# Performance work log

Measured on AMD Instinct MI355X. Metric: run time of the kernel, lower is better.

## Reference

```python
import jax, jax.numpy as jnp
import numpy as np


def setup_inputs() -> dict:
    key = jax.random.key(0)
    k1, k2 = jax.random.split(key)
    b, n, d = 8, 4096, 512
    num_codebooks, codebook_size = 1, 8192
    x = jax.random.normal(k1, (b, n, d), dtype=jnp.float32)
    embed = jax.random.normal(k2, (num_codebooks, codebook_size, d), dtype=jnp.float32)
    return {"x": x, "embed": embed}


def reference(x, embed):
    # Eval-mode forward of EuclideanCodebook (temperature 0 -> argmax of -cdist).
    # x: [b, n, d]; embed: [h, C, d] with h = num_codebooks = 1.
    b, n, d = x.shape
    h, C, _ = embed.shape
    flatten = x.reshape(h, b * n, d)                       # h * d packing (h=1)

    # dist = -cdist(flatten, embed): negative euclidean distance [h, N, C]
    x2 = jnp.sum(flatten * flatten, axis=-1, keepdims=True)   # [h, N, 1]
    e2 = jnp.sum(embed * embed, axis=-1)[:, None, :]          # [h, 1, C]
    xe = jnp.einsum('hnd,hcd->hnc', flatten, embed)           # [h, N, C]
    d2 = jnp.clip(x2 + e2 - 2.0 * xe, 0.0)
    dist = -jnp.sqrt(d2)                                      # [h, N, C]

    # gumbel_sample at temp 0 / eval -> straight argmax
    embed_ind_flat = jnp.argmax(dist, axis=-1)                # [h, N]

    # quantize = batched_embedding(embed_ind, embed): gather codes
    quantize = jnp.take_along_axis(embed, embed_ind_flat[..., None], axis=1)  # [h, N, d]

    # unpack + drop the codebook dim (needs_codebook_dim path)
    quantize = quantize.reshape(b, n, d)
    embed_ind = embed_ind_flat.reshape(b, n)
    dist = dist.reshape(h, b, n, C)  # dist keeps the codebook dim, as in source
    return quantize, embed_ind, dist
```

## Files before the change

kernel.cpp:

```cpp
#include <hip/hip_runtime.h>
#include <hip/hip_fp16.h>
#include <stdint.h>

typedef _Float16 f16x8 __attribute__((ext_vector_type(8)));
typedef _Float16 f16x4 __attribute__((ext_vector_type(4)));
typedef float    f32x4 __attribute__((ext_vector_type(4)));

static constexpr int NROWS = 32768;
static constexpr int NCODE = 8192;
static constexpr int DDIM  = 512;
static constexpr int BM = 256, BN = 256, BK = 64;
static constexpr int NBM = NROWS / BM;
static constexpr int NBN = NCODE / BN;
static constexpr int NPART = NBN * 2;

static constexpr size_t OFF_IND  = (size_t)NROWS * DDIM;
static constexpr size_t OFF_DIST = OFF_IND + NROWS;

static constexpr size_t WS_XH   = 0;
static constexpr size_t WS_XL   = WS_XH + (size_t)NROWS * DDIM * 2;
static constexpr size_t WS_EH   = WS_XL + (size_t)NROWS * DDIM * 2;
static constexpr size_t WS_EL   = WS_EH + (size_t)NCODE * DDIM * 2;
static constexpr size_t WS_X2   = WS_EL + (size_t)NCODE * DDIM * 2;
static constexpr size_t WS_E2   = WS_X2 + (size_t)NROWS * 4;
static constexpr size_t WS_PART = WS_E2 + (size_t)NCODE * 4;

__device__ inline void gload_lds16(const void* g, void* l) {
  __builtin_amdgcn_global_load_lds((const __attribute__((address_space(1))) void*)g,
                                   (__attribute__((address_space(3))) void*)l,
                                   16, 0, 0);
}

__global__ __launch_bounds__(128)
void prep_kernel(const float* __restrict__ x, const float* __restrict__ e,
                 _Float16* __restrict__ xh, _Float16* __restrict__ xl,
                 _Float16* __restrict__ eh, _Float16* __restrict__ el,
                 float* __restrict__ x2, float* __restrict__ e2)
{
  int bid = blockIdx.x;
  const float* src; _Float16 *dh, *dl; float* nrm;
  if (bid < NROWS) {
    src = x + (size_t)bid * DDIM;
    dh = xh + (size_t)bid * DDIM;  dl = xl + (size_t)bid * DDIM;
    nrm = x2 + bid;
  } else {
    int r = bid - NROWS;
    src = e + (size_t)r * DDIM;
    dh = eh + (size_t)r * DDIM;    dl = el + (size_t)r * DDIM;
    nrm = e2 + r;
  }
  int t = threadIdx.x;
  float4 v = reinterpret_cast<const float4*>(src)[t];
  double s = (double)v.x*v.x + (double)v.y*v.y + (double)v.z*v.z + (double)v.w*v.w;
  f16x4 h, l;
  h.x = (_Float16)v.x; l.x = (_Float16)(v.x - (float)h.x);
  h.y = (_Float16)v.y; l.y = (_Float16)(v.y - (float)h.y);
  h.z = (_Float16)v.z; l.z = (_Float16)(v.z - (float)h.z);
  h.w = (_Float16)v.w; l.w = (_Float16)(v.w - (float)h.w);
  reinterpret_cast<f16x4*>(dh)[t] = h;
  reinterpret_cast<f16x4*>(dl)[t] = l;
  #pragma unroll
  for (int m = 1; m < 64; m <<= 1) s += __shfl_xor(s, m);
  __shared__ double sh[2];
  if ((t & 63) == 0) sh[t >> 6] = s;
  __syncthreads();
  if (t == 0) nrm[0] = (float)(sh[0] + sh[1]);
}

__global__ __launch_bounds__(512, 2)
void dist_gemm_kernel(const _Float16* __restrict__ xh, const _Float16* __restrict__ xl,
                      const _Float16* __restrict__ eh, const _Float16* __restrict__ el,
                      const float* __restrict__ x2, const float* __restrict__ e2,
                      float* __restrict__ dist, float2* __restrict__ part)
{
  __shared__ _Float16 L[2][2][BM * BK];

  const int tid  = threadIdx.x;
  const int wid  = tid >> 6;
  const int lane = tid & 63;
  const int qwr  = wid >> 1;
  const int qwc  = wid & 1;

  const int flat = blockIdx.x;
  const int swz  = (flat & 7) * (int)(gridDim.x >> 3) + (flat >> 3);
  const int bm = swz >> 5;
  const int bn = swz & 31;
  const int R  = bm * BM;
  const int Cc = bn * BN;

  const int l3 = lane >> 3;
  const int l7 = lane & 7;
  const int srcslot = ((l7 ^ l3) << 4);

  auto STAGE = [&](int t, int nb) {
    const _Float16* As = (t < 16) ? xh : xl;
    const _Float16* Bs = (t < 8 || t >= 16) ? eh : el;
    const int k0b = (t & 7) * (BK * 2);
    #pragma unroll
    for (int h = 0; h < 2; ++h) {
      #pragma unroll
      for (int g = 0; g < 2; ++g) {
        const int r = h * 128 + g * 64 + wid * 8 + l3;
        gload_lds16((const char*)As + (size_t)(R + r) * (DDIM * 2) + k0b + srcslot,
                    &L[nb][0][(h * 128 + g * 64 + wid * 8) * BK]);
        gload_lds16((const char*)Bs + (size_t)(Cc + r) * (DDIM * 2) + k0b + srcslot,
                    &L[nb][1][(h * 128 + g * 64 + wid * 8) * BK]);
      }
    }
  };

  const int l15   = lane & 15;
  const int kslot = (lane >> 4) << 4;

  auto LDA = [&](f16x8 (&af)[2][2], int b, int mq) {
    #pragma unroll
    for (int m = 0; m < 2; ++m)
      #pragma unroll
      for (int ks = 0; ks < 2; ++ks) {
        const int row = mq * 128 + qwr * 32 + m * 16 + l15;
        const int kb  = (ks * 64 + kslot) ^ ((row & 7) << 4);
        af[m][ks] = *(const f16x8*)((const char*)&L[b][0][0] + row * 128 + kb);
      }
  };
  auto LDB = [&](f16x8 (&bf)[4][2], int b, int nq) {
    #pragma unroll
    for (int n = 0; n < 4; ++n)
      #pragma unroll
      for (int ks = 0; ks < 2; ++ks) {
        const int row = nq * 128 + qwc * 64 + n * 16 + l15;
        const int kb  = (ks * 64 + kslot) ^ ((row & 7) << 4);
        bf[n][ks] = *(const f16x8*)((const char*)&L[b][1][0] + row * 128 + kb);
      }
  };

  f32x4 acc[2][2][2][4] = {};

  auto MM = [&](f32x4 (&ac)[2][4], f16x8 (&af)[2][2], f16x8 (&bf)[4][2]) {
    #pragma unroll
    for (int m = 0; m < 2; ++m)
      #pragma unroll
      for (int n = 0; n < 4; ++n)
        #pragma unroll
        for (int ks = 0; ks < 2; ++ks)
          ac[m][n] = __builtin_amdgcn_mfma_f32_16x16x32_f16(af[m][ks], bf[n][ks], ac[m][n], 0, 0, 0);
  };

  STAGE(0, 0);
  asm volatile("s_waitcnt vmcnt(0)" ::: "memory");
  __builtin_amdgcn_s_barrier();

  for (int t = 0; t < 24; ++t) {
    const int b = t & 1;
    f16x8 af[2][2], bf0[4][2], bf1[4][2];

    if (t + 1 < 24) STAGE(t + 1, b ^ 1);
    LDA(af, b, 0);
    LDB(bf0, b, 0);
    __builtin_amdgcn_s_barrier();
    __builtin_amdgcn_s_setprio(1);
    MM(acc[0][0], af, bf0);
    __builtin_amdgcn_s_setprio(0);
    __builtin_amdgcn_s_barrier();

    LDB(bf1, b, 1);
    __builtin_amdgcn_s_barrier();
    __builtin_amdgcn_s_setprio(1);
    MM(acc[0][1], af, bf1);
    __builtin_amdgcn_s_setprio(0);
    __builtin_amdgcn_s_barrier();

    LDA(af, b, 1);
    __builtin_amdgcn_s_barrier();
    __builtin_amdgcn_s_setprio(1);
    MM(acc[1][0], af, bf0);
    __builtin_amdgcn_s_setprio(0);
    __builtin_amdgcn_s_barrier();

    __builtin_amdgcn_s_setprio(1);
    MM(acc[1][1], af, bf1);
    __builtin_amdgcn_s_setprio(0);
    asm volatile("s_waitcnt vmcnt(0)" ::: "memory");
    __builtin_amdgcn_s_barrier();
  }

  const int q    = lane >> 4;
  const int csub = lane & 15;

  float e2v[2][4];
  #pragma unroll
  for (int nq = 0; nq < 2; ++nq)
    #pragma unroll
    for (int n = 0; n < 4; ++n)
      e2v[nq][n] = e2[Cc + nq * 128 + qwc * 64 + n * 16 + csub];

  float bestv[16], besti[16];
  int rix = 0;
  #pragma unroll
  for (int mq = 0; mq < 2; ++mq)
    #pragma unroll
    for (int m = 0; m < 2; ++m)
      #pragma unroll
      for (int j = 0; j < 4; ++j, ++rix) {
        const int row = R + mq * 128 + qwr * 32 + m * 16 + q * 4 + j;
        const float xv = x2[row];
        float* drow = dist + (size_t)row * NCODE;
        float bv = -3.0e38f, bi = 0.0f;
        #pragma unroll
        for (int nq = 0; nq < 2; ++nq)
          #pragma unroll
          for (int n = 0; n < 4; ++n) {
            const int col = Cc + nq * 128 + qwc * 64 + n * 16 + csub;
            float xe = acc[mq][nq][m][n][j];
            float d2 = fmaxf((xv + e2v[nq][n]) - 2.0f * xe, 0.0f);
            float dv = -sqrtf(d2);
            drow[col] = dv;
            if (dv > bv) { bv = dv; bi = (float)col; }
          }
        bestv[rix] = bv;
        besti[rix] = bi;
      }

  #pragma unroll
  for (int msk = 1; msk < 16; msk <<= 1) {
    #pragma unroll
    for (int r = 0; r < 16; ++r) {
      float ov = __shfl_xor(bestv[r], msk);
      float oi = __shfl_xor(besti[r], msk);
      if (ov > bestv[r] || (ov == bestv[r] && oi < besti[r])) { bestv[r] = ov; besti[r] = oi; }
    }
  }
  if (csub == 0) {
    int rr = 0;
    #pragma unroll
    for (int mq = 0; mq < 2; ++mq)
      #pragma unroll
      for (int m = 0; m < 2; ++m)
        #pragma unroll
        for (int j = 0; j < 4; ++j, ++rr) {
          const int row = R + mq * 128 + qwr * 32 + m * 16 + q * 4 + j;
          part[(size_t)row * NPART + bn * 2 + qwc] = make_float2(bestv[rr], besti[rr]);
        }
  }
}

__global__ __launch_bounds__(64)
void reduce_gather_kernel(const float2* __restrict__ part, const float* __restrict__ embed,
                          float* __restrict__ quant, float* __restrict__ ind)
{
  const int row = blockIdx.x;
  const int l = threadIdx.x;
  float2 a = part[(size_t)row * NPART + l];
  float bv = a.x, bi = a.y;
  #pragma unroll
  for (int m = 1; m < 64; m <<= 1) {
    float ov = __shfl_xor(bv, m);
    float oi = __shfl_xor(bi, m);
    if (ov > bv || (ov == bv && oi < bi)) { bv = ov; bi = oi; }
  }
  if (l == 0) ind[row] = bi;
  const int idx = (int)bi;
  const float4* src = reinterpret_cast<const float4*>(embed + (size_t)idx * DDIM);
  float4* dst = reinterpret_cast<float4*>(quant + (size_t)row * DDIM);
  dst[l]      = src[l];
  dst[l + 64] = src[l + 64];
}

extern "C" void kernel_launch(void* const* d_in, const int* in_sizes, int n_in,
                              void* d_out, int out_size, void* d_ws, size_t ws_size,
                              hipStream_t stream) {
  const float* x     = (const float*)d_in[0];
  const float* embed = (const float*)d_in[1];

  char* ws = (char*)d_ws;
  _Float16* xh = (_Float16*)(ws + WS_XH);
  _Float16* xl = (_Float16*)(ws + WS_XL);
  _Float16* eh = (_Float16*)(ws + WS_EH);
  _Float16* el = (_Float16*)(ws + WS_EL);
  float*    x2 = (float*)(ws + WS_X2);
  float*    e2 = (float*)(ws + WS_E2);
  float2*   part = (float2*)(ws + WS_PART);

  float* quant = (float*)d_out;
  float* ind   = (float*)d_out + OFF_IND;
  float* dist  = (float*)d_out + OFF_DIST;

  prep_kernel<<<dim3(NROWS + NCODE), 128, 0, stream>>>(x, embed, xh, xl, eh, el, x2, e2);
  dist_gemm_kernel<<<dim3(NBM * NBN), 512, 0, stream>>>(xh, xl, eh, el, x2, e2, dist, part);
  reduce_gather_kernel<<<dim3(NROWS), 64, 0, stream>>>(part, embed, quant, ind);
}
```

Before: 1.115 ms.

## Split tile staging into quarters interleaved with MFMA phases, fine-grained vmcnt waits

The next K-tile's global-to-LDS load is split into four quarter loads, each issued between MFMA sub-blocks. Partial vmcnt waits replace the full drain at the end of each iteration, so copies overlap compute more evenly. The MFMA sub-block order is changed so each LDS quarter is consumed only after its load has landed. Launch bounds are relaxed to one block per SM and the dist stores become nontemporal, which gives more registers but risks lower occupancy and relies on the vmcnt counts being correct.

```diff
diff --git a/kernel.cpp b/kernel.cpp
--- a/kernel.cpp
+++ b/kernel.cpp
@@ -67,7 +67,7 @@
   if (t == 0) nrm[0] = (float)(sh[0] + sh[1]);
 }
 
-__global__ __launch_bounds__(512, 2)
+__global__ __launch_bounds__(512, 1)
 void dist_gemm_kernel(const _Float16* __restrict__ xh, const _Float16* __restrict__ xl,
                       const _Float16* __restrict__ eh, const _Float16* __restrict__ el,
                       const float* __restrict__ x2, const float* __restrict__ e2,
@@ -92,20 +92,19 @@
   const int l7 = lane & 7;
   const int srcslot = ((l7 ^ l3) << 4);
 
-  auto STAGE = [&](int t, int nb) {
-    const _Float16* As = (t < 16) ? xh : xl;
-    const _Float16* Bs = (t < 8 || t >= 16) ? eh : el;
+  auto STAGE_HALF = [&](int t, int nb, int half) {
+    const int ab = half & 1;
+    const int hh = half >> 1;
+    const _Float16* base;
+    size_t rowbase;
+    if (ab == 0) { base = (t < 16) ? xh : xl;              rowbase = (size_t)R;  }
+    else         { base = (t < 8 || t >= 16) ? eh : el;    rowbase = (size_t)Cc; }
     const int k0b = (t & 7) * (BK * 2);
     #pragma unroll
-    for (int h = 0; h < 2; ++h) {
-      #pragma unroll
-      for (int g = 0; g < 2; ++g) {
-        const int r = h * 128 + g * 64 + wid * 8 + l3;
-        gload_lds16((const char*)As + (size_t)(R + r) * (DDIM * 2) + k0b + srcslot,
-                    &L[nb][0][(h * 128 + g * 64 + wid * 8) * BK]);
-        gload_lds16((const char*)Bs + (size_t)(Cc + r) * (DDIM * 2) + k0b + srcslot,
-                    &L[nb][1][(h * 128 + g * 64 + wid * 8) * BK]);
-      }
+    for (int i = 0; i < 2; ++i) {
+      const int rr = hh * 128 + wid * 16 + i * 8;
+      gload_lds16((const char*)base + (rowbase + rr + l3) * (DDIM * 2) + k0b + srcslot,
+                  &L[nb][ab][rr * BK]);
     }
   };
 
@@ -145,41 +144,50 @@
           ac[m][n] = __builtin_amdgcn_mfma_f32_16x16x32_f16(af[m][ks], bf[n][ks], ac[m][n], 0, 0, 0);
   };
 
-  STAGE(0, 0);
-  asm volatile("s_waitcnt vmcnt(0)" ::: "memory");
-  __builtin_amdgcn_s_barrier();
+  STAGE_HALF(0, 0, 0);
+  STAGE_HALF(0, 0, 1);
+  STAGE_HALF(0, 0, 2);
+  STAGE_HALF(0, 0, 3);
 
   for (int t = 0; t < 24; ++t) {
     const int b = t & 1;
-    f16x8 af[2][2], bf0[4][2], bf1[4][2];
-
-    if (t + 1 < 24) STAGE(t + 1, b ^ 1);
-    LDA(af, b, 0);
+    f16x8 af0[2][2], af1[2][2], bf0[4][2], bf1[4][2];
+
+    if (t < 23) { STAGE_HALF(t + 1, b ^ 1, 0);
+                  asm volatile("s_waitcnt vmcnt(6)" ::: "memory"); }
+    else        { asm volatile("s_waitcnt vmcnt(4)" ::: "memory"); }
+    __builtin_amdgcn_s_barrier();
+    LDA(af0, b, 0);
     LDB(bf0, b, 0);
-    __builtin_amdgcn_s_barrier();
-    __builtin_amdgcn_s_setprio(1);
-    MM(acc[0][0], af, bf0);
-    __builtin_amdgcn_s_setprio(0);
-    __builtin_amdgcn_s_barrier();
-
+    __builtin_amdgcn_s_setprio(1);
+    MM(acc[0][0], af0, bf0);
+    __builtin_amdgcn_s_setprio(0);
+    __builtin_amdgcn_s_barrier();
+
+    if (t < 23) { STAGE_HALF(t + 1, b ^ 1, 1);
+                  asm volatile("s_waitcnt vmcnt(6)" ::: "memory"); }
+    else        { asm volatile("s_waitcnt vmcnt(2)" ::: "memory"); }
+    __builtin_amdgcn_s_barrier();
+    LDA(af1, b, 1);
+    __builtin_amdgcn_s_setprio(1);
+    MM(acc[1][0], af1, bf0);
+    __builtin_amdgcn_s_setprio(0);
+    __builtin_amdgcn_s_barrier();
+
+    if (t < 23) { STAGE_HALF(t + 1, b ^ 1, 2);
+                  asm volatile("s_waitcnt vmcnt(6)" ::: "memory"); }
+    else        { asm volatile("s_waitcnt vmcnt(0)" ::: "memory"); }
+    __builtin_amdgcn_s_barrier();
     LDB(bf1, b, 1);
-    __builtin_amdgcn_s_barrier();
-    __builtin_amdgcn_s_setprio(1);
-    MM(acc[0][1], af, bf1);
-    __builtin_amdgcn_s_setprio(0);
-    __builtin_amdgcn_s_barrier();
-
-    LDA(af, b, 1);
-    __builtin_amdgcn_s_barrier();
-    __builtin_amdgcn_s_setprio(1);
-    MM(acc[1][0], af, bf0);
-    __builtin_amdgcn_s_setprio(0);
-    __builtin_amdgcn_s_barrier();
-
-    __builtin_amdgcn_s_setprio(1);
-    MM(acc[1][1], af, bf1);
-    __builtin_amdgcn_s_setprio(0);
-    asm volatile("s_waitcnt vmcnt(0)" ::: "memory");
+    __builtin_amdgcn_s_setprio(1);
+    MM(acc[1][1], af1, bf1);
+    __builtin_amdgcn_s_setprio(0);
+    __builtin_amdgcn_s_barrier();
+
+    if (t < 23) STAGE_HALF(t + 1, b ^ 1, 3);
+    __builtin_amdgcn_s_setprio(1);
+    MM(acc[0][1], af0, bf1);
+    __builtin_amdgcn_s_setprio(0);
     __builtin_amdgcn_s_barrier();
   }
 
@@ -213,7 +221,7 @@
             float xe = acc[mq][nq][m][n][j];
             float d2 = fmaxf((xv + e2v[nq][n]) - 2.0f * xe, 0.0f);
             float dv = -sqrtf(d2);
-            drow[col] = dv;
+            __builtin_nontemporal_store(dv, &drow[col]);
             if (dv > bv) { bv = dv; bi = (float)col; }
           }
         bestv[rix] = bv;
```

Result: faster. 1.025 ms (-8.1%).
